# Optimization experiments

Measured on AMD Instinct MI355X. Metric: run time of the kernel, lower is better.

Reference implementation:

```python
import jax, jax.numpy as jnp
import numpy as np

N, D, H, L, E, P = 50000, 128, 128, 3, 640000, 100000


def setup_inputs() -> dict:
    key = jax.random.key(0)
    ks = jax.random.split(key, 10)
    x = jax.random.normal(ks[0], (N, D), dtype=jnp.float32)
    ei = jax.random.randint(ks[1], (2, E), 0, N, dtype=jnp.int64)
    pos = jax.random.randint(ks[2], (2, P), 0, N, dtype=jnp.int64)
    neg = jax.random.randint(ks[3], (2, P), 0, N, dtype=jnp.int64)
    # GCN weights: layer0 is [D,H], rest [H,H]; D==H so stack as [L,H,H]
    gcn_w = jax.random.normal(ks[4], (L, H, H), dtype=jnp.float32) / np.sqrt(H)
    gcn_b = jnp.zeros((L, H), dtype=jnp.float32)
    pred_w = jax.random.normal(ks[5], (H * L, 1), dtype=jnp.float32) / np.sqrt(H * L)
    pred_b = jnp.zeros((1,), dtype=jnp.float32)
    return {"x": x, "ei": ei, "pos": pos, "neg": neg,
            "gcn_w": gcn_w, "gcn_b": gcn_b, "pred_w": pred_w, "pred_b": pred_b}


def reference(x, ei, pos, neg, gcn_w, gcn_b, pred_w, pred_b):
    n = x.shape[0]
    loops = jnp.arange(n, dtype=ei.dtype)
    src = jnp.concatenate([ei[0], loops])  # self-loops (GCNConv default)
    dst = jnp.concatenate([ei[1], loops])
    deg = jax.ops.segment_sum(jnp.ones_like(dst, dtype=x.dtype), dst, num_segments=n)
    dinv = jax.lax.rsqrt(deg)  # deg >= 1 thanks to self-loops
    coef = (dinv[src] * dinv[dst])[:, None]  # [E+N, 1] symmetric norm

    embs = []
    h = x
    for i in range(gcn_w.shape[0]):
        hw = h @ gcn_w[i]                                   # [N, H]
        agg = jax.ops.segment_sum(hw[src] * coef, dst, num_segments=n)
        h = jax.nn.relu(agg + gcn_b[i])
        embs.append(h)
    z = jnp.concatenate(embs, axis=1)                        # [N, H*L]

    def logits(e):
        return (z[e[0]] * z[e[1]]) @ pred_w + pred_b         # [P, 1]

    pos_logit = logits(pos)
    neg_logit = logits(neg)
    # BCEWithLogitsLoss with targets [1...1, 0...0], mean reduction
    total = pos_logit.shape[0] + neg_logit.shape[0]
    loss = (jnp.sum(-jax.nn.log_sigmoid(pos_logit)) +
            jnp.sum(-jax.nn.log_sigmoid(-neg_logit))) / total
    return loss
```

## Files before the change

kernel.cpp:

```cpp
#include <hip/hip_runtime.h>
#include <hip/hip_bf16.h>

#define DD 128

typedef __attribute__((ext_vector_type(8))) short short8;
typedef __attribute__((ext_vector_type(4))) float f32x4;
typedef __attribute__((ext_vector_type(2))) float f32x2;

static __device__ __forceinline__ int gtid() {
    return blockIdx.x * blockDim.x + threadIdx.x;
}

static __device__ __forceinline__ ushort f2bfu(float f) {
    __hip_bfloat16 h = __float2bfloat16(f);
    return *reinterpret_cast<ushort*>(&h);
}

static __device__ __forceinline__ unsigned int fp8e(float f) {
    unsigned int s = (__float_as_uint(f) >> 31) << 7;
    float a = fabsf(f);
    if (a < 0.015625f) return s | (unsigned int)rintf(a * 512.0f);
    unsigned int u = __float_as_uint(a);
    u += 0x0007FFFFu + ((u >> 20) & 1u);
    unsigned int e8 = (u >> 23) - 120u;
    unsigned int m = (u >> 20) & 7u;
    if (e8 > 15u || (e8 == 15u && m == 7u)) return s | 0x7Eu;
    return s | (e8 << 3) | m;
}

static __device__ __forceinline__ float fp8d(unsigned int b) {
    unsigned int t = b & 0x7Fu;
    float v = (t >= 8u) ? __uint_as_float((t << 20) + 0x3C000000u)
                        : (float)t * 0.001953125f;
    return (b & 0x80u) ? -v : v;
}

static __device__ __forceinline__ unsigned int pk8x4(float a, float b, float c, float d) {
#if __has_builtin(__builtin_amdgcn_cvt_pk_fp8_f32)
    int v = __builtin_amdgcn_cvt_pk_fp8_f32(a, b, 0, false);
    v = __builtin_amdgcn_cvt_pk_fp8_f32(c, d, v, true);
    return (unsigned int)v;
#else
    return fp8e(a) | (fp8e(b) << 8) | (fp8e(c) << 16) | (fp8e(d) << 24);
#endif
}

static __device__ __forceinline__ unsigned int pk8x2(float a, float b) {
#if __has_builtin(__builtin_amdgcn_cvt_pk_fp8_f32)
    return (unsigned int)__builtin_amdgcn_cvt_pk_fp8_f32(a, b, 0, false);
#else
    return fp8e(a) | (fp8e(b) << 8);
#endif
}

static __device__ __forceinline__ void fp8x4_dec(unsigned int u, float* f) {
#if __has_builtin(__builtin_amdgcn_cvt_pk_f32_fp8)
    f32x2 lo = __builtin_amdgcn_cvt_pk_f32_fp8((int)u, false);
    f32x2 hi = __builtin_amdgcn_cvt_pk_f32_fp8((int)u, true);
    f[0] = lo[0]; f[1] = lo[1]; f[2] = hi[0]; f[3] = hi[1];
#else
    f[0] = fp8d(u & 0xFFu);
    f[1] = fp8d((u >> 8) & 0xFFu);
    f[2] = fp8d((u >> 16) & 0xFFu);
    f[3] = fp8d((u >> 24) & 0xFFu);
#endif
}


__global__ void count_kernel(int* __restrict__ counts, const int* __restrict__ dst, int e) {
    int i = gtid();
    if (i < e) atomicAdd(&counts[dst[i]], 1);
}

__global__ void dinv_kernel(float* __restrict__ dinv, const int* __restrict__ counts, int n) {
    int i = gtid();
    if (i < n) dinv[i] = rsqrtf(1.0f + (float)counts[i]);
}

__global__ __launch_bounds__(256) void scan_blocks(const int* __restrict__ counts,
                                                   int* __restrict__ rowptr,
                                                   int* __restrict__ partial, int n) {
    __shared__ int s[256];
    int i = blockIdx.x * 256 + threadIdx.x;
    int v = (i < n) ? counts[i] : 0;
    s[threadIdx.x] = v;
    __syncthreads();
    for (int off = 1; off < 256; off <<= 1) {
        int t = (threadIdx.x >= off) ? s[threadIdx.x - off] : 0;
        __syncthreads();
        s[threadIdx.x] += t;
        __syncthreads();
    }
    if (i < n) rowptr[i] = s[threadIdx.x] - v;
    if (threadIdx.x == 255) partial[blockIdx.x] = s[255];
}

__global__ __launch_bounds__(256) void scan_partials(int* __restrict__ partial,
                                                     int* __restrict__ partial2, int nb) {
    __shared__ int s[256];
    int v = (threadIdx.x < nb) ? partial[threadIdx.x] : 0;
    s[threadIdx.x] = v;
    __syncthreads();
    for (int off = 1; off < 256; off <<= 1) {
        int t = (threadIdx.x >= off) ? s[threadIdx.x - off] : 0;
        __syncthreads();
        s[threadIdx.x] += t;
        __syncthreads();
    }
    partial2[threadIdx.x] = s[threadIdx.x] - v;
}

__global__ __launch_bounds__(256) void add_offsets(int* __restrict__ rowptr,
                                                   int* __restrict__ cursor,
                                                   const int* __restrict__ partial2,
                                                   int n, int e) {
    int i = blockIdx.x * 256 + threadIdx.x;
    if (i < n) {
        int r = rowptr[i] + partial2[blockIdx.x];
        rowptr[i] = r;
        cursor[i] = r;
        if (i == n - 1) rowptr[n] = e;
    }
}

__global__ void fill_kernel(const int* __restrict__ ei, int* __restrict__ cursor,
                            int* __restrict__ csr_src, int e) {
    int i = gtid();
    if (i >= e) return;
    int s = ei[i];
    int d = ei[e + i];
    int pos = atomicAdd(&cursor[d], 1);
    csr_src[pos] = s;
}

__global__ void cvt_kernel(const float* __restrict__ x, __hip_bfloat16* __restrict__ xh, size_t m) {
    size_t i = (size_t)blockIdx.x * blockDim.x + threadIdx.x;
    if (i < m) xh[i] = __float2bfloat16(x[i]);
}

__global__ __launch_bounds__(256) void wpack_kernel(const float* __restrict__ gcn_w,
                                                    ushort* __restrict__ wfrag) {
    int tid = blockIdx.x * 256 + threadIdx.x;
    if (tid >= 3 * 4 * 8 * 64) return;
    int lane = tid & 63;
    int c = (tid >> 6) & 7;
    int s = (tid >> 9) & 3;
    int l = tid >> 11;
    const float* W = gcn_w + (size_t)l * 128 * 128;
    int col = c * 16 + (lane & 15);
    int k0 = s * 32 + (lane >> 4) * 8;
    ushort u[8];
#pragma unroll
    for (int j = 0; j < 8; ++j) {
        u[j] = f2bfu(W[(size_t)(k0 + j) * 128 + col]);
    }
    *reinterpret_cast<uint4*>(wfrag + (size_t)tid * 8) = *reinterpret_cast<const uint4*>(u);
}

__global__ __launch_bounds__(256) void gemm_mfma_kernel(
    const ushort* __restrict__ hsrc, int ld, const ushort* __restrict__ wfrag,
    unsigned char* __restrict__ outq, int ntiles) {
    int lane = threadIdx.x & 63;
    int wv = threadIdx.x >> 6;
    short8 b0[4], b1[4];
    int c0 = wv * 2;
#pragma unroll
    for (int s = 0; s < 4; ++s) {
        b0[s] = *reinterpret_cast<const short8*>(wfrag + ((size_t)(s * 8 + c0) * 64 + lane) * 8);
        b1[s] = *reinterpret_cast<const short8*>(wfrag + ((size_t)(s * 8 + c0 + 1) * 64 + lane) * 8);
    }
    int rlo = lane & 15;
    int kg = lane >> 4;
    for (int rt = blockIdx.x; rt < ntiles; rt += gridDim.x) {
        const ushort* ap = hsrc + (size_t)(rt * 16 + rlo) * ld + kg * 8;
        short8 a0 = *reinterpret_cast<const short8*>(ap);
        short8 a1 = *reinterpret_cast<const short8*>(ap + 32);
        short8 a2 = *reinterpret_cast<const short8*>(ap + 64);
        short8 a3 = *reinterpret_cast<const short8*>(ap + 96);
        f32x4 acc0 = {0.f, 0.f, 0.f, 0.f};
        f32x4 acc1 = {0.f, 0.f, 0.f, 0.f};
        acc0 = __builtin_amdgcn_mfma_f32_16x16x32_bf16(a0, b0[0], acc0, 0, 0, 0);
        acc1 = __builtin_amdgcn_mfma_f32_16x16x32_bf16(a0, b1[0], acc1, 0, 0, 0);
        acc0 = __builtin_amdgcn_mfma_f32_16x16x32_bf16(a1, b0[1], acc0, 0, 0, 0);
        acc1 = __builtin_amdgcn_mfma_f32_16x16x32_bf16(a1, b1[1], acc1, 0, 0, 0);
        acc0 = __builtin_amdgcn_mfma_f32_16x16x32_bf16(a2, b0[2], acc0, 0, 0, 0);
        acc1 = __builtin_amdgcn_mfma_f32_16x16x32_bf16(a2, b1[2], acc1, 0, 0, 0);
        acc0 = __builtin_amdgcn_mfma_f32_16x16x32_bf16(a3, b0[3], acc0, 0, 0, 0);
        acc1 = __builtin_amdgcn_mfma_f32_16x16x32_bf16(a3, b1[3], acc1, 0, 0, 0);
        int row0 = rt * 16 + kg * 4;
        unsigned char* orow = outq + (size_t)row0 * 128 + wv * 32 + rlo;
#pragma unroll
        for (int r = 0; r < 4; ++r) {
            unsigned int pk = pk8x2(acc0[r], acc1[r]);
            orow[(size_t)r * 128] = (unsigned char)(pk & 0xFFu);
            orow[(size_t)r * 128 + 16] = (unsigned char)((pk >> 8) & 0xFFu);
        }
    }
}

__global__ __launch_bounds__(256) void aggregate_kernel(
    const unsigned char* __restrict__ hwq, const int* __restrict__ rowptr,
    const int* __restrict__ csr_src, const float* __restrict__ dinv,
    const float* __restrict__ bias, const float* __restrict__ pwsl,
    ushort* __restrict__ zsl, unsigned char* __restrict__ zqsl,
    unsigned char* __restrict__ zqwsl, int n) {
    int gid = gtid();
    int row = gid >> 6;
    if (row >= n) return;
    int lane = threadIdx.x & 63;
    int g = lane >> 3;
    int c = lane & 7;
    int j0 = rowptr[row], j1 = rowptr[row + 1];
    float dr = dinv[row];
    float acc[16];
#pragma unroll
    for (int k = 0; k < 16; ++k) acc[k] = 0.f;
    for (int j = j0 + g; j < j1; j += 8) {
        int s = csr_src[j];
        float cf = dinv[s] * dr;
        uint4 v = *reinterpret_cast<const uint4*>(hwq + (size_t)s * 128 + c * 16);
        float f[16];
        fp8x4_dec(v.x, f);
        fp8x4_dec(v.y, f + 4);
        fp8x4_dec(v.z, f + 8);
        fp8x4_dec(v.w, f + 12);
#pragma unroll
        for (int k = 0; k < 16; ++k) acc[k] = fmaf(cf, f[k], acc[k]);
    }
#pragma unroll
    for (int k = 0; k < 16; ++k) {
        acc[k] += __shfl_xor(acc[k], 8);
        acc[k] += __shfl_xor(acc[k], 16);
        acc[k] += __shfl_xor(acc[k], 32);
    }
    float d2 = dr * dr;
    uint4 sv = *reinterpret_cast<const uint4*>(hwq + (size_t)row * 128 + c * 16);
    float sf[16];
    fp8x4_dec(sv.x, sf);
    fp8x4_dec(sv.y, sf + 4);
    fp8x4_dec(sv.z, sf + 8);
    fp8x4_dec(sv.w, sf + 12);
    float4 bb[4];
#pragma unroll
    for (int q = 0; q < 4; ++q)
        bb[q] = *reinterpret_cast<const float4*>(bias + c * 16 + q * 4);
    const float* bp = (const float*)bb;
#pragma unroll
    for (int k = 0; k < 16; ++k) {
        acc[k] = fmaxf(fmaf(d2, sf[k], acc[k]) + bp[k], 0.f);
    }

    if (g == 0) {
        unsigned int pk[8];
#pragma unroll
        for (int q = 0; q < 8; ++q) {
            pk[q] = (unsigned int)f2bfu(acc[2 * q]) | ((unsigned int)f2bfu(acc[2 * q + 1]) << 16);
        }
        ushort* zp = zsl + (size_t)row * 384 + c * 16;
        *reinterpret_cast<uint4*>(zp) = *reinterpret_cast<const uint4*>(pk);
        *reinterpret_cast<uint4*>(zp + 8) = *reinterpret_cast<const uint4*>(pk + 4);
    } else if (g == 1) {
        uint4 qq;
        qq.x = pk8x4(acc[0], acc[1], acc[2], acc[3]);
        qq.y = pk8x4(acc[4], acc[5], acc[6], acc[7]);
        qq.z = pk8x4(acc[8], acc[9], acc[10], acc[11]);
        qq.w = pk8x4(acc[12], acc[13], acc[14], acc[15]);
        *reinterpret_cast<uint4*>(zqsl + (size_t)row * 384 + c * 16) = qq;
    } else if (g == 2) {
        float w[16];
#pragma unroll
        for (int q = 0; q < 4; ++q) {
            float4 pv = *reinterpret_cast<const float4*>(pwsl + c * 16 + q * 4);
            const float* pp = (const float*)&pv;
#pragma unroll
            for (int t = 0; t < 4; ++t) w[q * 4 + t] = acc[q * 4 + t] * pp[t] * 8.0f;
        }
        uint4 ww;
        ww.x = pk8x4(w[0], w[1], w[2], w[3]);
        ww.y = pk8x4(w[4], w[5], w[6], w[7]);
        ww.z = pk8x4(w[8], w[9], w[10], w[11]);
        ww.w = pk8x4(w[12], w[13], w[14], w[15]);
        *reinterpret_cast<uint4*>(zqwsl + (size_t)row * 384 + c * 16) = ww;
    }
}

__global__ __launch_bounds__(256) void loss_mfma_kernel(
    const unsigned char* __restrict__ zq, const unsigned char* __restrict__ zqw,
    const int* __restrict__ pos, const int* __restrict__ neg,
    const float* __restrict__ pb, float* __restrict__ partialOut,
    int p, float inv_total) {
    __shared__ float red[4];
    int lane = threadIdx.x & 63;
    int wv = threadIdx.x >> 6;
    int pairBase = (blockIdx.x * 4 + wv) * 16;
    float term = 0.f;
    if (pairBase < 2 * p) {
        int m = lane & 15;
        int kg = lane >> 4;
        int pi = pairBase + m;
        int pic = (pi < 2 * p) ? pi : (2 * p - 1);
        bool isneg = (pic >= p);
        const int* pr = isneg ? neg : pos;
        int idx = isneg ? (pic - p) : pic;
        int a = pr[idx];
        int b = pr[p + idx];
        const long* pa = reinterpret_cast<const long*>(zq + (size_t)a * 384) + kg;
        const long* pbw = reinterpret_cast<const long*>(zqw + (size_t)b * 384) + kg;
        long av[12], bv[12];
#pragma unroll
        for (int s = 0; s < 12; ++s) av[s] = pa[s * 4];
#pragma unroll
        for (int s = 0; s < 12; ++s) bv[s] = pbw[s * 4];
        f32x4 acc = {0.f, 0.f, 0.f, 0.f};
#pragma unroll
        for (int s = 0; s < 12; ++s) {
            acc = __builtin_amdgcn_mfma_f32_16x16x32_fp8_fp8(av[s], bv[s], acc, 0, 0, 0);
        }
        bool isdiag = (lane >> 4) == ((lane & 15) >> 2);
        int r2 = lane & 3;
        float v = (r2 == 0) ? acc[0] : (r2 == 1) ? acc[1] : (r2 == 2) ? acc[2] : acc[3];
        if (isdiag && pi < 2 * p) {
            float logit = v * 0.125f + pb[0];
            float t = isneg ? logit : -logit;
            term = (fmaxf(t, 0.f) + log1pf(expf(-fabsf(t)))) * inv_total;
        }
    }
#pragma unroll
    for (int off = 1; off < 64; off <<= 1) term += __shfl_xor(term, off);
    if (lane == 0) red[wv] = term;
    __syncthreads();
    if (threadIdx.x == 0) partialOut[blockIdx.x] = red[0] + red[1] + red[2] + red[3];
}

__global__ __launch_bounds__(256) void loss_reduce_kernel(
    const float* __restrict__ partial, float* __restrict__ out, int m) {
    __shared__ float s[256];
    float a = 0.f;
    for (int i = threadIdx.x; i < m; i += 256) a += partial[i];
    s[threadIdx.x] = a;
    __syncthreads();
    for (int off = 128; off > 0; off >>= 1) {
        if (threadIdx.x < off) s[threadIdx.x] += s[threadIdx.x + off];
        __syncthreads();
    }
    if (threadIdx.x == 0) out[0] = s[0];
}

extern "C" void kernel_launch(void* const* d_in, const int* in_sizes, int n_in,
                              void* d_out, int out_size, void* d_ws, size_t ws_size,
                              hipStream_t stream) {
    const float* x      = (const float*)d_in[0];
    const int*   ei     = (const int*)d_in[1];
    const int*   pos    = (const int*)d_in[2];
    const int*   neg    = (const int*)d_in[3];
    const float* gcn_w  = (const float*)d_in[4];
    const float* gcn_b  = (const float*)d_in[5];
    const float* pred_w = (const float*)d_in[6];
    const float* pred_b = (const float*)d_in[7];
    float* out = (float*)d_out;

    const int n = in_sizes[0] / DD;
    const int e = in_sizes[1] / 2;
    const int p = in_sizes[2] / 2;
    const int nb = (n + 255) / 256;

    char* ws = (char*)d_ws;
    size_t off = 0;
    auto alloc = [&](size_t bytes) {
        void* ptr = ws + off;
        off += (bytes + 255) & ~(size_t)255;
        return ptr;
    };
    float* dinv      = (float*)alloc((size_t)n * 4);
    int*   counts    = (int*)alloc((size_t)n * 4);
    int*   rowptr    = (int*)alloc((size_t)(n + 1) * 4);
    int*   cursor    = (int*)alloc((size_t)n * 4);
    int*   partial   = (int*)alloc(256 * 4);
    int*   partial2  = (int*)alloc(256 * 4);
    float* lossPart  = (float*)alloc((size_t)4096 * 4);
    int*   csr_src   = (int*)alloc((size_t)e * 4);
    ushort* wfrag    = (ushort*)alloc((size_t)3 * 2048 * 8 * 2);
    ushort* xh = (ushort*)alloc((size_t)n * 128 * 2);
    unsigned char* hwq = (unsigned char*)alloc((size_t)n * 128);
    ushort* zh = (ushort*)alloc((size_t)n * 384 * 2);
    unsigned char* zq  = (unsigned char*)alloc((size_t)n * 384);
    unsigned char* zqw = (unsigned char*)alloc((size_t)n * 384);
    (void)ws_size;

    hipMemsetAsync(counts, 0, (size_t)n * 4, stream);
    hipMemsetAsync(d_out, 0, (size_t)out_size * 4, stream);

    count_kernel<<<(e + 255) / 256, 256, 0, stream>>>(counts, ei + e, e);
    dinv_kernel<<<nb, 256, 0, stream>>>(dinv, counts, n);
    scan_blocks<<<nb, 256, 0, stream>>>(counts, rowptr, partial, n);
    scan_partials<<<1, 256, 0, stream>>>(partial, partial2, nb);
    add_offsets<<<nb, 256, 0, stream>>>(rowptr, cursor, partial2, n, e);
    fill_kernel<<<(e + 255) / 256, 256, 0, stream>>>(ei, cursor, csr_src, e);

    cvt_kernel<<<(int)(((size_t)n * 128 + 255) / 256), 256, 0, stream>>>(
        x, (__hip_bfloat16*)xh, (size_t)n * 128);
    wpack_kernel<<<24, 256, 0, stream>>>(gcn_w, wfrag);

    const int ntiles = n / 16;
    const int aggBlocks = (n * 64 + 255) / 256;
    for (int l = 0; l < 3; ++l) {
        const ushort* hsrc = (l == 0) ? xh : (zh + (size_t)(l - 1) * 128);
        int ld = (l == 0) ? 128 : 384;
        gemm_mfma_kernel<<<ntiles, 256, 0, stream>>>(
            hsrc, ld, wfrag + (size_t)l * 2048 * 8, hwq, ntiles);
        aggregate_kernel<<<aggBlocks, 256, 0, stream>>>(
            hwq, rowptr, csr_src, dinv, gcn_b + (size_t)l * 128,
            pred_w + (size_t)l * 128,
            zh + (size_t)l * 128, zq + (size_t)l * 128, zqw + (size_t)l * 128, n);
    }

    float inv_total = 1.0f / (2.0f * (float)p);
    int lossBlocks = (2 * p + 63) / 64;
    loss_mfma_kernel<<<lossBlocks, 256, 0, stream>>>(
        zq, zqw, pos, neg, pred_b, lossPart, p, inv_total);
    loss_reduce_kernel<<<1, 256, 0, stream>>>(lossPart, out, lossBlocks);
}
```

Before: 288.2 us.

## Reorder GCN layers to aggregate before GEMM and fuse bias/relu/quantize into GEMM

Each GCN layer now aggregates neighbors first (A·H) and then multiplies by W, using linearity, instead of GEMM then aggregate. Layer 0 gathers bf16 input rows and later layers gather fp8 z rows directly. Bias, ReLU, fp8 quantization and the pred_w-scaled copy move into the GEMM epilogue, which drops the bf16 z buffer and the fp8 hw intermediate. The gather reads fp8/bf16 data of similar width, so the main saving is fewer writes and passes. It also adds a nontemporal store in the CSR fill and removes the output memset. Precision changes slightly because later layers aggregate fp8-quantized activations rather than bf16 ones.

Result: no change. 285.7 us (-0.9%).

```diff
diff --git a/kernel.cpp b/kernel.cpp
--- a/kernel.cpp
+++ b/kernel.cpp
@@ -130,7 +130,7 @@
     int s = ei[i];
     int d = ei[e + i];
     int pos = atomicAdd(&cursor[d], 1);
-    csr_src[pos] = s;
+    __builtin_nontemporal_store(s, &csr_src[pos]);
 }
 
 __global__ void cvt_kernel(const float* __restrict__ x, __hip_bfloat16* __restrict__ xh, size_t m) {
@@ -157,9 +157,105 @@
     *reinterpret_cast<uint4*>(wfrag + (size_t)tid * 8) = *reinterpret_cast<const uint4*>(u);
 }
 
+
+__global__ __launch_bounds__(256) void aggregate_bf16_kernel(
+    const ushort* __restrict__ src, const int* __restrict__ rowptr,
+    const int* __restrict__ csr_src, const float* __restrict__ dinv,
+    ushort* __restrict__ aggh, int n) {
+    int gid = gtid();
+    int row = gid >> 6;
+    if (row >= n) return;
+    int lane = threadIdx.x & 63;
+    int g = lane >> 4;
+    int c = lane & 15;
+    int j0 = rowptr[row], j1 = rowptr[row + 1];
+    float dr = dinv[row];
+    float acc[8] = {0.f, 0.f, 0.f, 0.f, 0.f, 0.f, 0.f, 0.f};
+    for (int j = j0 + g; j < j1; j += 4) {
+        int s = csr_src[j];
+        float cf = dinv[s] * dr;
+        uint4 v = *reinterpret_cast<const uint4*>(src + (size_t)s * 128 + c * 8);
+        const unsigned int* u = (const unsigned int*)&v;
+#pragma unroll
+        for (int q = 0; q < 4; ++q) {
+            acc[2 * q] = fmaf(cf, __uint_as_float(u[q] << 16), acc[2 * q]);
+            acc[2 * q + 1] = fmaf(cf, __uint_as_float(u[q] & 0xffff0000u), acc[2 * q + 1]);
+        }
+    }
+#pragma unroll
+    for (int k = 0; k < 8; ++k) {
+        acc[k] += __shfl_xor(acc[k], 16);
+        acc[k] += __shfl_xor(acc[k], 32);
+    }
+    float d2 = dr * dr;
+    uint4 sv = *reinterpret_cast<const uint4*>(src + (size_t)row * 128 + c * 8);
+    const unsigned int* su = (const unsigned int*)&sv;
+#pragma unroll
+    for (int q = 0; q < 4; ++q) {
+        acc[2 * q] = fmaf(d2, __uint_as_float(su[q] << 16), acc[2 * q]);
+        acc[2 * q + 1] = fmaf(d2, __uint_as_float(su[q] & 0xffff0000u), acc[2 * q + 1]);
+    }
+    if (g == 0) {
+        unsigned int pk[4];
+#pragma unroll
+        for (int q = 0; q < 4; ++q) {
+            pk[q] = (unsigned int)f2bfu(acc[2 * q]) | ((unsigned int)f2bfu(acc[2 * q + 1]) << 16);
+        }
+        *reinterpret_cast<uint4*>(aggh + (size_t)row * 128 + c * 8) =
+            *reinterpret_cast<const uint4*>(pk);
+    }
+}
+
+__global__ __launch_bounds__(256) void aggregate_fp8_kernel(
+    const unsigned char* __restrict__ srcq, const int* __restrict__ rowptr,
+    const int* __restrict__ csr_src, const float* __restrict__ dinv,
+    ushort* __restrict__ aggh, int n) {
+    int gid = gtid();
+    int row = gid >> 6;
+    if (row >= n) return;
+    int lane = threadIdx.x & 63;
+    int g = lane >> 4;
+    int c = lane & 15;
+    int j0 = rowptr[row], j1 = rowptr[row + 1];
+    float dr = dinv[row];
+    float acc[8] = {0.f, 0.f, 0.f, 0.f, 0.f, 0.f, 0.f, 0.f};
+    for (int j = j0 + g; j < j1; j += 4) {
+        int s = csr_src[j];
+        float cf = dinv[s] * dr;
+        uint2 v = *reinterpret_cast<const uint2*>(srcq + (size_t)s * 384 + c * 8);
+        float f[8];
+        fp8x4_dec(v.x, f);
+        fp8x4_dec(v.y, f + 4);
+#pragma unroll
+        for (int k = 0; k < 8; ++k) acc[k] = fmaf(cf, f[k], acc[k]);
+    }
+#pragma unroll
+    for (int k = 0; k < 8; ++k) {
+        acc[k] += __shfl_xor(acc[k], 16);
+        acc[k] += __shfl_xor(acc[k], 32);
+    }
+    float d2 = dr * dr;
+    uint2 sv = *reinterpret_cast<const uint2*>(srcq + (size_t)row * 384 + c * 8);
+    float sf[8];
+    fp8x4_dec(sv.x, sf);
+    fp8x4_dec(sv.y, sf + 4);
+#pragma unroll
+    for (int k = 0; k < 8; ++k) acc[k] = fmaf(d2, sf[k], acc[k]);
+    if (g == 0) {
+        unsigned int pk[4];
+#pragma unroll
+        for (int q = 0; q < 4; ++q) {
+            pk[q] = (unsigned int)f2bfu(acc[2 * q]) | ((unsigned int)f2bfu(acc[2 * q + 1]) << 16);
+        }
+        *reinterpret_cast<uint4*>(aggh + (size_t)row * 128 + c * 8) =
+            *reinterpret_cast<const uint4*>(pk);
+    }
+}
+
 __global__ __launch_bounds__(256) void gemm_mfma_kernel(
-    const ushort* __restrict__ hsrc, int ld, const ushort* __restrict__ wfrag,
-    unsigned char* __restrict__ outq, int ntiles) {
+    const ushort* __restrict__ aggh, const ushort* __restrict__ wfrag,
+    const float* __restrict__ bias, const float* __restrict__ pwsl,
+    unsigned char* __restrict__ zq_sl, unsigned char* __restrict__ zqw_sl, int ntiles) {
     int lane = threadIdx.x & 63;
     int wv = threadIdx.x >> 6;
     short8 b0[4], b1[4];
@@ -171,8 +267,12 @@
     }
     int rlo = lane & 15;
     int kg = lane >> 4;
+    int col0 = wv * 32 + rlo;
+    int col1 = col0 + 16;
+    float bias0 = bias[col0], bias1 = bias[col1];
+    float pw0 = pwsl[col0] * 8.0f, pw1 = pwsl[col1] * 8.0f;
     for (int rt = blockIdx.x; rt < ntiles; rt += gridDim.x) {
-        const ushort* ap = hsrc + (size_t)(rt * 16 + rlo) * ld + kg * 8;
+        const ushort* ap = aggh + (size_t)(rt * 16 + rlo) * 128 + kg * 8;
         short8 a0 = *reinterpret_cast<const short8*>(ap);
         short8 a1 = *reinterpret_cast<const short8*>(ap + 32);
         short8 a2 = *reinterpret_cast<const short8*>(ap + 64);
@@ -188,99 +288,19 @@
         acc0 = __builtin_amdgcn_mfma_f32_16x16x32_bf16(a3, b0[3], acc0, 0, 0, 0);
         acc1 = __builtin_amdgcn_mfma_f32_16x16x32_bf16(a3, b1[3], acc1, 0, 0, 0);
         int row0 = rt * 16 + kg * 4;
-        unsigned char* orow = outq + (size_t)row0 * 128 + wv * 32 + rlo;
 #pragma unroll
         for (int r = 0; r < 4; ++r) {
-            unsigned int pk = pk8x2(acc0[r], acc1[r]);
-            orow[(size_t)r * 128] = (unsigned char)(pk & 0xFFu);
-            orow[(size_t)r * 128 + 16] = (unsigned char)((pk >> 8) & 0xFFu);
-        }
-    }
-}
-
-__global__ __launch_bounds__(256) void aggregate_kernel(
-    const unsigned char* __restrict__ hwq, const int* __restrict__ rowptr,
-    const int* __restrict__ csr_src, const float* __restrict__ dinv,
-    const float* __restrict__ bias, const float* __restrict__ pwsl,
-    ushort* __restrict__ zsl, unsigned char* __restrict__ zqsl,
-    unsigned char* __restrict__ zqwsl, int n) {
-    int gid = gtid();
-    int row = gid >> 6;
-    if (row >= n) return;
-    int lane = threadIdx.x & 63;
-    int g = lane >> 3;
-    int c = lane & 7;
-    int j0 = rowptr[row], j1 = rowptr[row + 1];
-    float dr = dinv[row];
-    float acc[16];
-#pragma unroll
-    for (int k = 0; k < 16; ++k) acc[k] = 0.f;
-    for (int j = j0 + g; j < j1; j += 8) {
-        int s = csr_src[j];
-        float cf = dinv[s] * dr;
-        uint4 v = *reinterpret_cast<const uint4*>(hwq + (size_t)s * 128 + c * 16);
-        float f[16];
-        fp8x4_dec(v.x, f);
-        fp8x4_dec(v.y, f + 4);
-        fp8x4_dec(v.z, f + 8);
-        fp8x4_dec(v.w, f + 12);
-#pragma unroll
-        for (int k = 0; k < 16; ++k) acc[k] = fmaf(cf, f[k], acc[k]);
-    }
-#pragma unroll
-    for (int k = 0; k < 16; ++k) {
-        acc[k] += __shfl_xor(acc[k], 8);
-        acc[k] += __shfl_xor(acc[k], 16);
-        acc[k] += __shfl_xor(acc[k], 32);
-    }
-    float d2 = dr * dr;
-    uint4 sv = *reinterpret_cast<const uint4*>(hwq + (size_t)row * 128 + c * 16);
-    float sf[16];
-    fp8x4_dec(sv.x, sf);
-    fp8x4_dec(sv.y, sf + 4);
-    fp8x4_dec(sv.z, sf + 8);
-    fp8x4_dec(sv.w, sf + 12);
-    float4 bb[4];
-#pragma unroll
-    for (int q = 0; q < 4; ++q)
-        bb[q] = *reinterpret_cast<const float4*>(bias + c * 16 + q * 4);
-    const float* bp = (const float*)bb;
-#pragma unroll
-    for (int k = 0; k < 16; ++k) {
-        acc[k] = fmaxf(fmaf(d2, sf[k], acc[k]) + bp[k], 0.f);
-    }
-
-    if (g == 0) {
-        unsigned int pk[8];
-#pragma unroll
-        for (int q = 0; q < 8; ++q) {
-            pk[q] = (unsigned int)f2bfu(acc[2 * q]) | ((unsigned int)f2bfu(acc[2 * q + 1]) << 16);
-        }
-        ushort* zp = zsl + (size_t)row * 384 + c * 16;
-        *reinterpret_cast<uint4*>(zp) = *reinterpret_cast<const uint4*>(pk);
-        *reinterpret_cast<uint4*>(zp + 8) = *reinterpret_cast<const uint4*>(pk + 4);
-    } else if (g == 1) {
-        uint4 qq;
-        qq.x = pk8x4(acc[0], acc[1], acc[2], acc[3]);
-        qq.y = pk8x4(acc[4], acc[5], acc[6], acc[7]);
-        qq.z = pk8x4(acc[8], acc[9], acc[10], acc[11]);
-        qq.w = pk8x4(acc[12], acc[13], acc[14], acc[15]);
-        *reinterpret_cast<uint4*>(zqsl + (size_t)row * 384 + c * 16) = qq;
-    } else if (g == 2) {
-        float w[16];
-#pragma unroll
-        for (int q = 0; q < 4; ++q) {
-            float4 pv = *reinterpret_cast<const float4*>(pwsl + c * 16 + q * 4);
-            const float* pp = (const float*)&pv;
-#pragma unroll
-            for (int t = 0; t < 4; ++t) w[q * 4 + t] = acc[q * 4 + t] * pp[t] * 8.0f;
-        }
-        uint4 ww;
-        ww.x = pk8x4(w[0], w[1], w[2], w[3]);
-        ww.y = pk8x4(w[4], w[5], w[6], w[7]);
-        ww.z = pk8x4(w[8], w[9], w[10], w[11]);
-        ww.w = pk8x4(w[12], w[13], w[14], w[15]);
-        *reinterpret_cast<uint4*>(zqwsl + (size_t)row * 384 + c * 16) = ww;
+            float v0 = fmaxf(acc0[r] + bias0, 0.f);
+            float v1 = fmaxf(acc1[r] + bias1, 0.f);
+            unsigned int q = pk8x2(v0, v1);
+            unsigned char* zr = zq_sl + (size_t)(row0 + r) * 384 + col0;
+            zr[0] = (unsigned char)(q & 0xFFu);
+            zr[16] = (unsigned char)((q >> 8) & 0xFFu);
+            unsigned int w = pk8x2(v0 * pw0, v1 * pw1);
+            unsigned char* wr = zqw_sl + (size_t)(row0 + r) * 384 + col0;
+            wr[0] = (unsigned char)(w & 0xFFu);
+            wr[16] = (unsigned char)((w >> 8) & 0xFFu);
+        }
     }
 }
 
@@ -380,15 +400,13 @@
     float* lossPart  = (float*)alloc((size_t)4096 * 4);
     int*   csr_src   = (int*)alloc((size_t)e * 4);
     ushort* wfrag    = (ushort*)alloc((size_t)3 * 2048 * 8 * 2);
-    ushort* xh = (ushort*)alloc((size_t)n * 128 * 2);
-    unsigned char* hwq = (unsigned char*)alloc((size_t)n * 128);
-    ushort* zh = (ushort*)alloc((size_t)n * 384 * 2);
+    ushort* xh   = (ushort*)alloc((size_t)n * 128 * 2);
+    ushort* aggh = (ushort*)alloc((size_t)n * 128 * 2);
     unsigned char* zq  = (unsigned char*)alloc((size_t)n * 384);
     unsigned char* zqw = (unsigned char*)alloc((size_t)n * 384);
     (void)ws_size;
 
     hipMemsetAsync(counts, 0, (size_t)n * 4, stream);
-    hipMemsetAsync(d_out, 0, (size_t)out_size * 4, stream);
 
     count_kernel<<<(e + 255) / 256, 256, 0, stream>>>(counts, ei + e, e);
     dinv_kernel<<<nb, 256, 0, stream>>>(dinv, counts, n);
@@ -404,14 +422,17 @@
     const int ntiles = n / 16;
     const int aggBlocks = (n * 64 + 255) / 256;
     for (int l = 0; l < 3; ++l) {
-        const ushort* hsrc = (l == 0) ? xh : (zh + (size_t)(l - 1) * 128);
-        int ld = (l == 0) ? 128 : 384;
+        if (l == 0) {
+            aggregate_bf16_kernel<<<aggBlocks, 256, 0, stream>>>(
+                xh, rowptr, csr_src, dinv, aggh, n);
+        } else {
+            aggregate_fp8_kernel<<<aggBlocks, 256, 0, stream>>>(
+                zq + (size_t)(l - 1) * 128, rowptr, csr_src, dinv, aggh, n);
+        }
         gemm_mfma_kernel<<<ntiles, 256, 0, stream>>>(
-            hsrc, ld, wfrag + (size_t)l * 2048 * 8, hwq, ntiles);
-        aggregate_kernel<<<aggBlocks, 256, 0, stream>>>(
-            hwq, rowptr, csr_src, dinv, gcn_b + (size_t)l * 128,
-            pred_w + (size_t)l * 128,
-            zh + (size_t)l * 128, zq + (size_t)l * 128, zqw + (size_t)l * 128, n);
+            aggh, wfrag + (size_t)l * 2048 * 8,
+            gcn_b + (size_t)l * 128, pred_w + (size_t)l * 128,
+            zq + (size_t)l * 128, zqw + (size_t)l * 128, ntiles);
     }
 
     float inv_total = 1.0f / (2.0f * (float)p);
```
